# Performance work log

Hardware: AMD Instinct MI355X
Metric: run time of the kernel (lower is better)

The kernel has to match this reference:

```python
import jax, jax.numpy as jnp
import numpy as np


def _blur_kernel():
    # make_kernel([1,3,3,1]) -> outer product, normalized; * upsample_factor**2 (=4)
    k = np.array([1.0, 3.0, 3.0, 1.0], dtype=np.float32)
    k2 = np.outer(k, k)
    k2 /= k2.sum()
    k2 *= 4.0
    return jnp.asarray(k2)  # [4,4]


def setup_inputs() -> dict:
    key = jax.random.key(0)
    ks = jax.random.split(key, 6)
    B, Cin, Cout, H, W = 8, 128, 128, 128, 128
    style_dim, sd = 512, 32
    lin_out = Cin * (sd // 2) * (sd // 2)  # 128*16*16 = 32768
    return {
        "x": jax.random.normal(ks[0], (B, Cin, H, W), jnp.float32),
        "style": jax.random.normal(ks[1], (B, style_dim), jnp.float32),
        "weight": jax.random.normal(ks[2], (Cout, Cin, 3, 3), jnp.float32),
        "lin_w": jax.random.normal(ks[3], (lin_out, style_dim), jnp.float32),
        "lin_b": jnp.ones((lin_out,), jnp.float32),  # bias_init=1
        "convw_w": jax.random.normal(ks[4], (Cout, Cin, 3, 3), jnp.float32),
        "convw_b": jnp.zeros((Cout,), jnp.float32),
        "convb_w": jax.random.normal(ks[5], (Cout, Cin, 3, 3), jnp.float32),
        "convb_b": jnp.zeros((Cout,), jnp.float32),
    }


DN = ('NCHW', 'OIHW', 'NCHW')


def reference(x, style, weight, lin_w, lin_b, convw_w, convw_b, convb_w, convb_b):
    B, Cin, H, W = x.shape
    Cout, K = weight.shape[0], weight.shape[2]
    scale = 1.0 / np.sqrt(Cin * K * K)  # equalized-lr scale, fan_in = Cin*K*K
    w = scale * weight  # [Cout, Cin, K, K]; identical per-sample -> plain conv

    # F.conv_transpose2d(stride=2, padding=0) == dilated conv with flipped kernel
    out = jax.lax.conv_general_dilated(
        x, jnp.flip(w, (2, 3)), (1, 1), [(K - 1, K - 1)] * 2,
        lhs_dilation=(2, 2), dimension_numbers=DN)  # [B, Cout, 2H+1, 2W+1]

    # upfirdn2d blur with pad=(1,1): depthwise conv with flipped 4x4 kernel
    bk = _blur_kernel()
    bw = jnp.tile(jnp.flip(bk, (0, 1))[None, None], (Cout, 1, 1, 1))  # [Cout,1,4,4]
    out = jax.lax.conv_general_dilated(
        out, bw, (1, 1), [(1, 1), (1, 1)], feature_group_count=Cout,
        dimension_numbers=DN)  # [B, Cout, 2H, 2W]

    # InstanceNorm2d(affine=False), eps=1e-5, biased variance
    mu = out.mean((2, 3), keepdims=True)
    var = out.var((2, 3), keepdims=True)
    out = (out - mu) * jax.lax.rsqrt(var + 1e-5)
    Ho, Wo = out.shape[2], out.shape[3]

    # spatial_modulation_shared: EqualLinear (fused_lrelu) + View
    half = int(round(np.sqrt(lin_w.shape[0] // Cin)))  # spatial_dim // 2
    sd = 2 * half
    lscale = 1.0 / np.sqrt(style.shape[1])
    s = style @ (lin_w * lscale).T
    s = jax.nn.leaky_relu(s + lin_b, 0.2) * np.sqrt(2.0)  # fused_leaky_relu
    smap = s.reshape(B, Cin, half, half)
    # nn.Upsample(scale_factor=2, mode='nearest')
    smap = jnp.repeat(jnp.repeat(smap, 2, axis=2), 2, axis=3)  # [B,Cin,sd,sd]

    # two EqualConv2d(Cin, Cout, 3, padding=1)
    cscale = 1.0 / np.sqrt(Cin * 9)
    sw = jax.lax.conv_general_dilated(smap, convw_w * cscale, (1, 1),
                                      [(1, 1), (1, 1)], dimension_numbers=DN)
    sw = sw + convw_b[None, :, None, None]
    sb = jax.lax.conv_general_dilated(smap, convb_w * cscale, (1, 1),
                                      [(1, 1), (1, 1)], dimension_numbers=DN)
    sb = sb + convb_b[None, :, None, None]

    # F.interpolate(mode='nearest') to (Ho, Wo)
    hi = jnp.arange(Ho) * sd // Ho
    wi = jnp.arange(Wo) * sd // Wo
    sw = sw[:, :, hi][:, :, :, wi]
    sb = sb[:, :, hi][:, :, :, wi]

    return out * (1.0 + 0.3 * sw) + 0.3 * sb
```

## Files before the change

### kernel.cpp

```cpp
#include <hip/hip_runtime.h>
#include <cstdint>

#define SCALE_MAIN 0.029462782549439483f
#define LSCALE     0.044194173824159223f
#define CSCALE     0.029462782549439483f

typedef __attribute__((ext_vector_type(8))) short bf16x8;
typedef __attribute__((ext_vector_type(4))) float f32x4;
typedef __attribute__((ext_vector_type(4))) unsigned int u32x4;

static __device__ __forceinline__ float lrelu_s2(float v) {
  return (v > 0.f ? v : 0.2f * v) * 1.4142135623730951f;
}

static __device__ __forceinline__ unsigned short f2bf(float f) {
  unsigned int u = __builtin_bit_cast(unsigned int, f);
  u += 0x7FFFu + ((u >> 16) & 1u);
  return (unsigned short)(u >> 16);
}

__global__ __launch_bounds__(256) void keffb_kernel(const float* __restrict__ weight,
                                                    short* __restrict__ kb) {
  int idx = blockIdx.x * 256 + threadIdx.x;
  if (idx >= 128 * 128 * 36) return;
  int tap = idx % 9;
  int tmp = idx / 9;
  int par = tmp & 3;
  int cc  = tmp >> 2;
  int co = cc >> 7, ci = cc & 127;
  int ph = par >> 1, pw = par & 1;
  int a = tap / 3, b = tap % 3;
  int th = ph ? 3 - 2 * a : 2 - 2 * a;
  int tw = pw ? 3 - 2 * b : 2 - 2 * b;
  const float k4[4] = {1.f, 3.f, 3.f, 1.f};
  const float* wp = weight + cc * 9;
  float acc = 0.f;
  #pragma unroll
  for (int u = 0; u < 4; ++u) {
    int m = th - 1 + u;
    if (m < 0 || m > 2) continue;
    #pragma unroll
    for (int v = 0; v < 4; ++v) {
      int n = tw - 1 + v;
      if (n < 0 || n > 2) continue;
      acc += (k4[3 - u] * k4[3 - v] * (1.f / 16.f)) * wp[m * 3 + n];
    }
  }
  kb[(((par * 144) + tap * 16 + (ci >> 3)) * 128 + co) * 8 + (ci & 7)] =
      (short)f2bf(acc * SCALE_MAIN);
}

__global__ __launch_bounds__(256) void xpose_kernel(const float* __restrict__ x,
                                                    unsigned short* __restrict__ xt) {
  int y = blockIdx.x, b = blockIdx.y;
  __shared__ unsigned short tl[128 * 134];
  int t = threadIdx.x;
  #pragma unroll 4
  for (int i = 0; i < 16; ++i) {
    int c = t + i * 256;
    int ci = c >> 5, x4 = c & 31;
    f32x4 v = *(const f32x4*)(x + (size_t)(b * 128 + ci) * 16384 + y * 128 + x4 * 4);
    unsigned int* dst = (unsigned int*)(tl + ci * 134 + x4 * 4);
    dst[0] = (unsigned int)f2bf(v.x) | ((unsigned int)f2bf(v.y) << 16);
    dst[1] = (unsigned int)f2bf(v.z) | ((unsigned int)f2bf(v.w) << 16);
  }
  __syncthreads();
  #pragma unroll 2
  for (int i = 0; i < 8; ++i) {
    int c = t + i * 256;
    int xcol = c >> 4, sub = c & 15;
    unsigned short u[8];
    #pragma unroll
    for (int j = 0; j < 8; ++j) u[j] = tl[(sub * 8 + j) * 134 + xcol];
    u32x4 o;
    o.x = (unsigned int)u[0] | ((unsigned int)u[1] << 16);
    o.y = (unsigned int)u[2] | ((unsigned int)u[3] << 16);
    o.z = (unsigned int)u[4] | ((unsigned int)u[5] << 16);
    o.w = (unsigned int)u[6] | ((unsigned int)u[7] << 16);
    *(u32x4*)(xt + ((size_t)(b * 128 + y) * 128 + xcol) * 128 + sub * 8) = o;
  }
}

__global__ __launch_bounds__(256) void style_kernel(const float* __restrict__ style,
                                                    const float* __restrict__ lin_w,
                                                    const float* __restrict__ lin_b,
                                                    float* __restrict__ smap) {
  int wid = threadIdx.x >> 6, lane = threadIdx.x & 63;
  int gw = blockIdx.x * 4 + wid;
  const float4* st4 = (const float4*)style;
  float s[8][8];
  #pragma unroll
  for (int b = 0; b < 8; ++b) {
    float4 a0 = st4[b * 128 + lane * 2];
    float4 a1 = st4[b * 128 + lane * 2 + 1];
    s[b][0] = a0.x; s[b][1] = a0.y; s[b][2] = a0.z; s[b][3] = a0.w;
    s[b][4] = a1.x; s[b][5] = a1.y; s[b][6] = a1.z; s[b][7] = a1.w;
  }
  for (int rr = 0; rr < 16; ++rr) {
    int j = gw * 16 + rr;
    const float4* wp = (const float4*)(lin_w + (size_t)j * 512);
    float4 w0 = wp[lane * 2], w1 = wp[lane * 2 + 1];
    float acc[8];
    #pragma unroll
    for (int b = 0; b < 8; ++b) {
      acc[b] = w0.x * s[b][0] + w0.y * s[b][1] + w0.z * s[b][2] + w0.w * s[b][3]
             + w1.x * s[b][4] + w1.y * s[b][5] + w1.z * s[b][6] + w1.w * s[b][7];
    }
    #pragma unroll
    for (int m = 32; m; m >>= 1) {
      #pragma unroll
      for (int b = 0; b < 8; ++b) acc[b] += __shfl_xor(acc[b], m, 64);
    }
    if (lane == 0) {
      float bias = lin_b[j];
      #pragma unroll
      for (int b = 0; b < 8; ++b)
        smap[(size_t)b * 32768 + j] = lrelu_s2(acc[b] * LSCALE + bias);
    }
  }
}

__global__ __launch_bounds__(256) void modconv_kernel(const float* __restrict__ smap,
    const float* __restrict__ cw_w, const float* __restrict__ cw_b,
    const float* __restrict__ cb_w, const float* __restrict__ cb_b,
    float* __restrict__ sw, float* __restrict__ sb) {
  int co = blockIdx.x, b = blockIdx.y;
  int t = threadIdx.x;
  __shared__ float wts[2][1152];
  __shared__ float smc[8192];
  for (int i = t; i < 1152; i += 256) {
    wts[0][i] = cw_w[(size_t)co * 1152 + i];
    wts[1][i] = cb_w[(size_t)co * 1152 + i];
  }
  int qh = t >> 4, qw = t & 15;
  float aw[4] = {0, 0, 0, 0}, ab2[4] = {0, 0, 0, 0};
  for (int cc = 0; cc < 4; ++cc) {
    __syncthreads();
    const f32x4* sp4 = (const f32x4*)(smap + (size_t)b * 32768 + cc * 8192);
    f32x4* smc4 = (f32x4*)smc;
    #pragma unroll
    for (int i = 0; i < 8; ++i) smc4[t + i * 256] = sp4[t + i * 256];
    __syncthreads();
    for (int ci = 0; ci < 32; ++ci) {
      const float* sm = smc + ci * 256;
      float pt[3][3];
      #pragma unroll
      for (int dy = 0; dy < 3; ++dy)
      #pragma unroll
      for (int dx = 0; dx < 3; ++dx) {
        int yy = qh - 1 + dy, xx = qw - 1 + dx;
        pt[dy][dx] = (yy >= 0 && yy < 16 && xx >= 0 && xx < 16) ? sm[yy * 16 + xx] : 0.f;
      }
      const float* w0p = &wts[0][(cc * 32 + ci) * 9];
      const float* w1p = &wts[1][(cc * 32 + ci) * 9];
      #pragma unroll
      for (int kh = 0; kh < 3; ++kh)
      #pragma unroll
      for (int kw = 0; kw < 3; ++kw) {
        float wwv = w0p[kh * 3 + kw], wbv = w1p[kh * 3 + kw];
        #pragma unroll
        for (int q = 0; q < 4; ++q) {
          int ey = (q >> 1) - 1 + kh;
          int ex = (q & 1) - 1 + kw;
          int py = (ey < 0) ? 0 : (ey < 2 ? 1 : 2);
          int px = (ex < 0) ? 0 : (ex < 2 ? 1 : 2);
          float v = pt[py][px];
          aw[q] += wwv * v;
          ab2[q] += wbv * v;
        }
      }
    }
  }
  float bw = cw_b[co], bb = cb_b[co];
  #pragma unroll
  for (int q = 0; q < 4; ++q) {
    int h = 2 * qh + (q >> 1), w = 2 * qw + (q & 1);
    size_t o = ((size_t)(b * 128 + co) * 32 + h) * 32 + w;
    sw[o] = aw[q] * CSCALE + bw;
    sb[o] = ab2[q] * CSCALE + bb;
  }
}

#define LOADSTEP(S, AV, BV)                                                      \
  {                                                                              \
    int tap_ = (S) >> 2;                                                         \
    int ta_ = (tap_ * 11) >> 5, tb_ = tap_ - ta_ * 3;                            \
    const char* ab_ = abase + (ta_ * 66 + tb_) * 272 + ((S) & 3) * 64;           \
    _Pragma("unroll")                                                            \
    for (int mf = 0; mf < 4; ++mf) AV[mf] = *(const bf16x8*)(ab_ + mf * 4352);   \
    _Pragma("unroll")                                                            \
    for (int nf = 0; nf < 8; ++nf) BV[nf] = kbv[bbase + (S) * 512 + nf * 16];    \
  }
#define MFMASTEP(AV, BV)                                                         \
  _Pragma("unroll")                                                              \
  for (int nf = 0; nf < 8; ++nf)                                                 \
  _Pragma("unroll")                                                              \
  for (int mf = 0; mf < 4; ++mf)                                                 \
    acc[mf][nf] = __builtin_amdgcn_mfma_f32_16x16x32_bf16(AV[mf], BV[nf], acc[mf][nf], 0, 0, 0);

template <int BF16OUT>
__global__ __launch_bounds__(256, 2) void main_kernel(const unsigned short* __restrict__ xt,
    const short* __restrict__ kb, float* __restrict__ out,
    unsigned short* __restrict__ xout, float* __restrict__ partial) {
  __shared__ __align__(16) char smem[53856];
  int xh = blockIdx.x, y0 = blockIdx.y, b = blockIdx.z;
  int x0 = xh * 64;
  int t = threadIdx.x;
  int lane = t & 63, p = t >> 6;
  int m15 = lane & 15, ksub = lane >> 4;
  int ph = p >> 1, pw = p & 1;

  const char* xtc = (const char*)xt;
  for (int c = t; c < 3168; c += 256) {
    int spos = c >> 4, sub = c & 15;
    int aa = spos / 66, cc2 = spos - aa * 66;
    int y = y0 - 1 + aa, xg = x0 - 1 + cc2;
    f32x4 v = {0.f, 0.f, 0.f, 0.f};
    if ((unsigned)y < 128u && (unsigned)xg < 128u)
      v = *(const f32x4*)(xtc + ((size_t)((b * 128 + y) * 128 + xg)) * 256 + sub * 16);
    *(f32x4*)(smem + spos * 272 + sub * 16) = v;
  }
  __syncthreads();

  const bf16x8* kbv = (const bf16x8*)kb;
  int bbase = p * 18432 + ksub * 128 + m15;
  const char* abase = smem + m15 * 272 + ksub * 16;

  f32x4 acc[4][8];
  #pragma unroll
  for (int i = 0; i < 4; ++i)
  #pragma unroll
  for (int j = 0; j < 8; ++j) acc[i][j] = (f32x4){0.f, 0.f, 0.f, 0.f};

  bf16x8 avA[4], bvA[8], avB[4], bvB[8];
  LOADSTEP(0, avA, bvA)
  for (int s = 0; s < 36; s += 2) {
    LOADSTEP(s + 1, avB, bvB)
    MFMASTEP(avA, bvA)
    if (s + 2 < 36) LOADSTEP(s + 2, avA, bvA)
    MFMASTEP(avB, bvB)
  }

  __syncthreads();
  float* eps = (float*)smem;
  int co16 = t & 15, slotid = t >> 4;
  int ph2 = slotid >> 3, w16 = slotid & 7;
  #pragma unroll
  for (int r2 = 0; r2 < 4; ++r2) {
    #pragma unroll
    for (int e = 0; e < 2; ++e) {
      int nf = r2 * 2 + e;
      float s1 = 0.f, s2 = 0.f;
      #pragma unroll
      for (int mf = 0; mf < 4; ++mf)
      #pragma unroll
      for (int r = 0; r < 4; ++r) {
        int xx = mf * 16 + ksub * 4 + r;
        float v = acc[mf][nf][r];
        eps[((e * 2 + ph) * 128 + 2 * xx + pw) * 17 + m15] = v;
        s1 += v; s2 += v * v;
      }
      s1 += __shfl_xor(s1, 16, 64); s1 += __shfl_xor(s1, 32, 64);
      s2 += __shfl_xor(s2, 16, 64); s2 += __shfl_xor(s2, 32, 64);
      if (lane < 16) {
        int co = nf * 16 + lane;
        size_t pidx = (((((size_t)b * 128 + co) * 128 + y0) * 2 + xh) * 4 + p) * 2;
        partial[pidx] = s1; partial[pidx + 1] = s2;
      }
    }
    __syncthreads();
    #pragma unroll
    for (int e = 0; e < 2; ++e) {
      int nf = r2 * 2 + e;
      int co = nf * 16 + co16;
      int h = 2 * y0 + ph2;
      float vv[16];
      #pragma unroll
      for (int i = 0; i < 16; ++i)
        vv[i] = eps[((e * 2 + ph2) * 128 + w16 * 16 + i) * 17 + co16];
      size_t obase = ((size_t)(b * 128 + co) * 256 + h) * 256 + xh * 128 + w16 * 16;
      if (BF16OUT) {
        u32x4 o0, o1;
        o0.x = (unsigned int)f2bf(vv[0])  | ((unsigned int)f2bf(vv[1])  << 16);
        o0.y = (unsigned int)f2bf(vv[2])  | ((unsigned int)f2bf(vv[3])  << 16);
        o0.z = (unsigned int)f2bf(vv[4])  | ((unsigned int)f2bf(vv[5])  << 16);
        o0.w = (unsigned int)f2bf(vv[6])  | ((unsigned int)f2bf(vv[7])  << 16);
        o1.x = (unsigned int)f2bf(vv[8])  | ((unsigned int)f2bf(vv[9])  << 16);
        o1.y = (unsigned int)f2bf(vv[10]) | ((unsigned int)f2bf(vv[11]) << 16);
        o1.z = (unsigned int)f2bf(vv[12]) | ((unsigned int)f2bf(vv[13]) << 16);
        o1.w = (unsigned int)f2bf(vv[14]) | ((unsigned int)f2bf(vv[15]) << 16);
        *(u32x4*)(xout + obase) = o0;
        *(u32x4*)(xout + obase + 8) = o1;
      } else {
        #pragma unroll
        for (int i = 0; i < 4; ++i) {
          f32x4 o4 = {vv[i * 4], vv[i * 4 + 1], vv[i * 4 + 2], vv[i * 4 + 3]};
          *(f32x4*)(out + obase + i * 4) = o4;
        }
      }
    }
    __syncthreads();
  }
}

__global__ __launch_bounds__(256) void stats_kernel(const float* __restrict__ partial,
                                                    float* __restrict__ stats) {
  int bc = blockIdx.x;
  int t = threadIdx.x;
  float s1 = 0.f, s2 = 0.f;
  for (int j = t; j < 1024; j += 256) {
    s1 += partial[(size_t)bc * 2048 + 2 * j];
    s2 += partial[(size_t)bc * 2048 + 2 * j + 1];
  }
  #pragma unroll
  for (int m = 32; m; m >>= 1) { s1 += __shfl_xor(s1, m, 64); s2 += __shfl_xor(s2, m, 64); }
  __shared__ float rb[8];
  if ((t & 63) == 0) { rb[(t >> 6) * 2] = s1; rb[(t >> 6) * 2 + 1] = s2; }
  __syncthreads();
  if (t == 0) {
    float a1 = rb[0] + rb[2] + rb[4] + rb[6];
    float a2 = rb[1] + rb[3] + rb[5] + rb[7];
    float mean = a1 * (1.f / 65536.f);
    float var = a2 * (1.f / 65536.f) - mean * mean;
    stats[bc * 2] = mean;
    stats[bc * 2 + 1] = rsqrtf(var + 1e-5f);
  }
}

__global__ __launch_bounds__(256) void final_kernel(float* __restrict__ out,
    const float* __restrict__ sw, const float* __restrict__ sb,
    const float* __restrict__ stats) {
  unsigned int tid = blockIdx.x * 256 + threadIdx.x;
  unsigned int e = tid * 4;
  unsigned int w = e & 255u;
  unsigned int h = (e >> 8) & 255u;
  unsigned int bc = e >> 16;
  float mean = stats[bc * 2], rstd = stats[bc * 2 + 1];
  unsigned int sidx = (bc * 32 + (h >> 3)) * 32 + (w >> 3);
  float f1 = (1.f + 0.3f * sw[sidx]) * rstd;
  float f0 = 0.3f * sb[sidx] - mean * f1;
  float4 v = *(float4*)(out + e);
  v.x = v.x * f1 + f0;
  v.y = v.y * f1 + f0;
  v.z = v.z * f1 + f0;
  v.w = v.w * f1 + f0;
  *(float4*)(out + e) = v;
}

__global__ __launch_bounds__(256) void final_bf16_kernel(float* __restrict__ out,
    const unsigned short* __restrict__ xout,
    const float* __restrict__ sw, const float* __restrict__ sb,
    const float* __restrict__ stats) {
  unsigned int tid = blockIdx.x * 256 + threadIdx.x;
  unsigned int e = tid * 8;
  unsigned int w = e & 255u;
  unsigned int h = (e >> 8) & 255u;
  unsigned int bc = e >> 16;
  float mean = stats[bc * 2], rstd = stats[bc * 2 + 1];
  unsigned int sidx = (bc * 32 + (h >> 3)) * 32 + (w >> 3);
  float f1 = (1.f + 0.3f * sw[sidx]) * rstd;
  float f0 = 0.3f * sb[sidx] - mean * f1;
  u32x4 uv = *(const u32x4*)(xout + e);
  float o[8];
  #pragma unroll
  for (int j = 0; j < 4; ++j) {
    unsigned int word = uv[j];
    float lo = __builtin_bit_cast(float, word << 16);
    float hi = __builtin_bit_cast(float, word & 0xFFFF0000u);
    o[2 * j]     = lo * f1 + f0;
    o[2 * j + 1] = hi * f1 + f0;
  }
  f32x4 a = {o[0], o[1], o[2], o[3]}, c = {o[4], o[5], o[6], o[7]};
  *(f32x4*)(out + e) = a;
  *(f32x4*)(out + e + 4) = c;
}

extern "C" void kernel_launch(void* const* d_in, const int* in_sizes, int n_in,
                              void* d_out, int out_size, void* d_ws, size_t ws_size,
                              hipStream_t stream) {
  const float* x      = (const float*)d_in[0];
  const float* style  = (const float*)d_in[1];
  const float* weight = (const float*)d_in[2];
  const float* lin_w  = (const float*)d_in[3];
  const float* lin_b  = (const float*)d_in[4];
  const float* cw_w   = (const float*)d_in[5];
  const float* cw_b   = (const float*)d_in[6];
  const float* cb_w   = (const float*)d_in[7];
  const float* cb_b   = (const float*)d_in[8];
  float* out = (float*)d_out;
  char* ws = (char*)d_ws;

  short*          kbb   = (short*)(ws);
  unsigned short* xt    = (unsigned short*)(ws + 1179648);
  float*          smap  = (float*)(ws + 34734080);
  float*          swb   = (float*)(ws + 35782656);
  float*          sbb   = (float*)(ws + 39976960);
  float*          part  = (float*)(ws + 44171264);
  float*          stats = (float*)(ws + 52559872);
  unsigned short* xout  = (unsigned short*)(ws + 52568064);
  bool bigws = ws_size >= (size_t)186785792;

  keffb_kernel<<<dim3(2304), dim3(256), 0, stream>>>(weight, kbb);
  xpose_kernel<<<dim3(128, 8), dim3(256), 0, stream>>>(x, xt);
  style_kernel<<<dim3(512), dim3(256), 0, stream>>>(style, lin_w, lin_b, smap);
  modconv_kernel<<<dim3(128, 8), dim3(256), 0, stream>>>(smap, cw_w, cw_b, cb_w, cb_b, swb, sbb);
  if (bigws) {
    main_kernel<1><<<dim3(2, 128, 8), dim3(256), 0, stream>>>(xt, kbb, out, xout, part);
    stats_kernel<<<dim3(1024), dim3(256), 0, stream>>>(part, stats);
    final_bf16_kernel<<<dim3(32768), dim3(256), 0, stream>>>(out, xout, swb, sbb, stats);
  } else {
    main_kernel<0><<<dim3(2, 128, 8), dim3(256), 0, stream>>>(xt, kbb, out, nullptr, part);
    stats_kernel<<<dim3(1024), dim3(256), 0, stream>>>(part, stats);
    final_kernel<<<dim3(65536), dim3(256), 0, stream>>>(out, swb, sbb, stats);
  }
}
```

Baseline: 393.7 us.

## Rewrite style modulation conv as polyphase bf16 MFMA GEMM and prioritize MFMA issue

```diff
diff --git a/kernel.cpp b/kernel.cpp
--- a/kernel.cpp
+++ b/kernel.cpp
@@ -50,6 +50,38 @@
       (short)f2bf(acc * SCALE_MAIN);
 }
 
+__global__ __launch_bounds__(256) void kb2_kernel(const float* __restrict__ cw_w,
+                                                  const float* __restrict__ cb_w,
+                                                  short* __restrict__ kb2) {
+  int idx = blockIdx.x * 256 + threadIdx.x;
+  if (idx >= 524288) return;
+  int j   = idx & 7;
+  int co  = (idx >> 3) & 255;
+  int kc  = (idx >> 11) & 63;
+  int par = idx >> 17;
+  int k = kc * 8 + j;
+  int t2 = k >> 7, ci = k & 127;
+  int dy2 = t2 >> 1, dx2 = t2 & 1;
+  int ph = par >> 1, pw = par & 1;
+  const float* wsrc = (co < 128)
+      ? cw_w + ((size_t)co * 128 + ci) * 9
+      : cb_w + ((size_t)(co - 128) * 128 + ci) * 9;
+  float acc = 0.f;
+  #pragma unroll
+  for (int kh = 0; kh < 3; ++kh) {
+    bool okh = dy2 == 0 ? (ph == 0 ? kh == 0 : kh <= 1)
+                        : (ph == 0 ? kh >= 1 : kh == 2);
+    if (!okh) continue;
+    #pragma unroll
+    for (int kw = 0; kw < 3; ++kw) {
+      bool okw = dx2 == 0 ? (pw == 0 ? kw == 0 : kw <= 1)
+                          : (pw == 0 ? kw >= 1 : kw == 2);
+      if (okw) acc += wsrc[kh * 3 + kw];
+    }
+  }
+  kb2[idx] = (short)f2bf(acc * CSCALE);
+}
+
 __global__ __launch_bounds__(256) void xpose_kernel(const float* __restrict__ x,
                                                     unsigned short* __restrict__ xt) {
   int y = blockIdx.x, b = blockIdx.y;
@@ -84,7 +116,7 @@
 __global__ __launch_bounds__(256) void style_kernel(const float* __restrict__ style,
                                                     const float* __restrict__ lin_w,
                                                     const float* __restrict__ lin_b,
-                                                    float* __restrict__ smap) {
+                                                    unsigned short* __restrict__ smap_bf) {
   int wid = threadIdx.x >> 6, lane = threadIdx.x & 63;
   int gw = blockIdx.x * 4 + wid;
   const float4* st4 = (const float4*)style;
@@ -113,71 +145,79 @@
     }
     if (lane == 0) {
       float bias = lin_b[j];
+      int ci = j >> 8, sp = j & 255;
       #pragma unroll
       for (int b = 0; b < 8; ++b)
-        smap[(size_t)b * 32768 + j] = lrelu_s2(acc[b] * LSCALE + bias);
-    }
-  }
-}
-
-__global__ __launch_bounds__(256) void modconv_kernel(const float* __restrict__ smap,
-    const float* __restrict__ cw_w, const float* __restrict__ cw_b,
-    const float* __restrict__ cb_w, const float* __restrict__ cb_b,
-    float* __restrict__ sw, float* __restrict__ sb) {
-  int co = blockIdx.x, b = blockIdx.y;
-  int t = threadIdx.x;
-  __shared__ float wts[2][1152];
-  __shared__ float smc[8192];
-  for (int i = t; i < 1152; i += 256) {
-    wts[0][i] = cw_w[(size_t)co * 1152 + i];
-    wts[1][i] = cb_w[(size_t)co * 1152 + i];
-  }
-  int qh = t >> 4, qw = t & 15;
-  float aw[4] = {0, 0, 0, 0}, ab2[4] = {0, 0, 0, 0};
-  for (int cc = 0; cc < 4; ++cc) {
-    __syncthreads();
-    const f32x4* sp4 = (const f32x4*)(smap + (size_t)b * 32768 + cc * 8192);
-    f32x4* smc4 = (f32x4*)smc;
-    #pragma unroll
-    for (int i = 0; i < 8; ++i) smc4[t + i * 256] = sp4[t + i * 256];
-    __syncthreads();
-    for (int ci = 0; ci < 32; ++ci) {
-      const float* sm = smc + ci * 256;
-      float pt[3][3];
-      #pragma unroll
-      for (int dy = 0; dy < 3; ++dy)
-      #pragma unroll
-      for (int dx = 0; dx < 3; ++dx) {
-        int yy = qh - 1 + dy, xx = qw - 1 + dx;
-        pt[dy][dx] = (yy >= 0 && yy < 16 && xx >= 0 && xx < 16) ? sm[yy * 16 + xx] : 0.f;
+        smap_bf[(size_t)(b * 256 + sp) * 128 + ci] =
+            f2bf(lrelu_s2(acc[b] * LSCALE + bias));
+    }
+  }
+}
+
+__global__ __launch_bounds__(512, 2) void modconv_kernel(
+    const unsigned short* __restrict__ smap_bf, const short* __restrict__ kb2,
+    const float* __restrict__ cw_b, const float* __restrict__ cb_b,
+    float* __restrict__ swp) {
+  extern __shared__ __align__(16) char dsm[];
+  int par = blockIdx.x, b = blockIdx.y;
+  int ph = par >> 1, pw = par & 1;
+  int t = threadIdx.x, lane = t & 63, w = t >> 6;
+  int q = w >> 1, ch = w & 1;
+  int m15 = lane & 15, ksub = lane >> 4;
+
+  for (int c = t; c < 4624; c += 512) {
+    int s = c >> 4, cch = c & 15;
+    int rr = s / 17, cc = s - rr * 17;
+    int gr = rr - 1 + ph, gc = cc - 1 + pw;
+    u32x4 v = {0u, 0u, 0u, 0u};
+    if ((unsigned)gr < 16u && (unsigned)gc < 16u)
+      v = *(const u32x4*)(smap_bf + ((size_t)(b * 256 + gr * 16 + gc) * 128 + cch * 8));
+    int phys = (cch + s) & 15;
+    *(u32x4*)(dsm + s * 256 + phys * 16) = v;
+  }
+  __syncthreads();
+
+  const bf16x8* kbv = (const bf16x8*)kb2;
+  f32x4 acc[4][8];
+  #pragma unroll
+  for (int i = 0; i < 4; ++i)
+  #pragma unroll
+  for (int j = 0; j < 8; ++j) acc[i][j] = (f32x4){0.f, 0.f, 0.f, 0.f};
+
+  for (int s = 0; s < 16; ++s) {
+    int t2 = s >> 2, dy2 = t2 >> 1, dx2 = t2 & 1;
+    int cch = (s & 3) * 4 + ksub;
+    bf16x8 av[4];
+    #pragma unroll
+    for (int mf = 0; mf < 4; ++mf) {
+      int i = q * 4 + mf;
+      int ssp = (i + dy2) * 17 + (m15 + dx2);
+      int phys = (cch + ssp) & 15;
+      av[mf] = *(const bf16x8*)(dsm + ssp * 256 + phys * 16);
+    }
+    #pragma unroll
+    for (int nf = 0; nf < 8; ++nf) {
+      bf16x8 bv = kbv[(size_t)((par * 64 + s * 4 + ksub) * 256 + ch * 128 + nf * 16 + m15)];
+      #pragma unroll
+      for (int mf = 0; mf < 4; ++mf)
+        acc[mf][nf] = __builtin_amdgcn_mfma_f32_16x16x32_bf16(av[mf], bv, acc[mf][nf], 0, 0, 0);
+    }
+  }
+
+  int jbase = ksub * 4;
+  #pragma unroll
+  for (int nf = 0; nf < 8; ++nf) {
+    int co = ch * 128 + nf * 16 + m15;
+    float bias = (co < 128) ? cw_b[co] : cb_b[co - 128];
+    #pragma unroll
+    for (int mf = 0; mf < 4; ++mf) {
+      int i = q * 4 + mf;
+      #pragma unroll
+      for (int r = 0; r < 4; ++r) {
+        int px = i * 16 + jbase + r;
+        swp[((size_t)(b * 256 + co) * 4 + par) * 256 + px] = acc[mf][nf][r] + bias;
       }
-      const float* w0p = &wts[0][(cc * 32 + ci) * 9];
-      const float* w1p = &wts[1][(cc * 32 + ci) * 9];
-      #pragma unroll
-      for (int kh = 0; kh < 3; ++kh)
-      #pragma unroll
-      for (int kw = 0; kw < 3; ++kw) {
-        float wwv = w0p[kh * 3 + kw], wbv = w1p[kh * 3 + kw];
-        #pragma unroll
-        for (int q = 0; q < 4; ++q) {
-          int ey = (q >> 1) - 1 + kh;
-          int ex = (q & 1) - 1 + kw;
-          int py = (ey < 0) ? 0 : (ey < 2 ? 1 : 2);
-          int px = (ex < 0) ? 0 : (ex < 2 ? 1 : 2);
-          float v = pt[py][px];
-          aw[q] += wwv * v;
-          ab2[q] += wbv * v;
-        }
-      }
-    }
-  }
-  float bw = cw_b[co], bb = cb_b[co];
-  #pragma unroll
-  for (int q = 0; q < 4; ++q) {
-    int h = 2 * qh + (q >> 1), w = 2 * qw + (q & 1);
-    size_t o = ((size_t)(b * 128 + co) * 32 + h) * 32 + w;
-    sw[o] = aw[q] * CSCALE + bw;
-    sb[o] = ab2[q] * CSCALE + bb;
+    }
   }
 }
 
@@ -192,11 +232,13 @@
     for (int nf = 0; nf < 8; ++nf) BV[nf] = kbv[bbase + (S) * 512 + nf * 16];    \
   }
 #define MFMASTEP(AV, BV)                                                         \
+  __builtin_amdgcn_s_setprio(1);                                                 \
   _Pragma("unroll")                                                              \
   for (int nf = 0; nf < 8; ++nf)                                                 \
   _Pragma("unroll")                                                              \
   for (int mf = 0; mf < 4; ++mf)                                                 \
-    acc[mf][nf] = __builtin_amdgcn_mfma_f32_16x16x32_bf16(AV[mf], BV[nf], acc[mf][nf], 0, 0, 0);
+    acc[mf][nf] = __builtin_amdgcn_mfma_f32_16x16x32_bf16(AV[mf], BV[nf], acc[mf][nf], 0, 0, 0); \
+  __builtin_amdgcn_s_setprio(0);
 
 template <int BF16OUT>
 __global__ __launch_bounds__(256, 2) void main_kernel(const unsigned short* __restrict__ xt,
@@ -328,17 +370,21 @@
 }
 
 __global__ __launch_bounds__(256) void final_kernel(float* __restrict__ out,
-    const float* __restrict__ sw, const float* __restrict__ sb,
-    const float* __restrict__ stats) {
+    const float* __restrict__ swp, const float* __restrict__ stats) {
   unsigned int tid = blockIdx.x * 256 + threadIdx.x;
   unsigned int e = tid * 4;
   unsigned int w = e & 255u;
   unsigned int h = (e >> 8) & 255u;
   unsigned int bc = e >> 16;
+  unsigned int b = bc >> 7, co = bc & 127u;
   float mean = stats[bc * 2], rstd = stats[bc * 2 + 1];
-  unsigned int sidx = (bc * 32 + (h >> 3)) * 32 + (w >> 3);
-  float f1 = (1.f + 0.3f * sw[sidx]) * rstd;
-  float f0 = 0.3f * sb[sidx] - mean * f1;
+  unsigned int r32 = h >> 3, c32 = w >> 3;
+  unsigned int par = (r32 & 1u) * 2 + (c32 & 1u);
+  unsigned int px = (r32 >> 1) * 16 + (c32 >> 1);
+  float msw = swp[((size_t)(b * 256 + co) * 4 + par) * 256 + px];
+  float msb = swp[((size_t)(b * 256 + 128 + co) * 4 + par) * 256 + px];
+  float f1 = (1.f + 0.3f * msw) * rstd;
+  float f0 = 0.3f * msb - mean * f1;
   float4 v = *(float4*)(out + e);
   v.x = v.x * f1 + f0;
   v.y = v.y * f1 + f0;
@@ -349,17 +395,21 @@
 
 __global__ __launch_bounds__(256) void final_bf16_kernel(float* __restrict__ out,
     const unsigned short* __restrict__ xout,
-    const float* __restrict__ sw, const float* __restrict__ sb,
-    const float* __restrict__ stats) {
+    const float* __restrict__ swp, const float* __restrict__ stats) {
   unsigned int tid = blockIdx.x * 256 + threadIdx.x;
   unsigned int e = tid * 8;
   unsigned int w = e & 255u;
   unsigned int h = (e >> 8) & 255u;
   unsigned int bc = e >> 16;
+  unsigned int b = bc >> 7, co = bc & 127u;
   float mean = stats[bc * 2], rstd = stats[bc * 2 + 1];
-  unsigned int sidx = (bc * 32 + (h >> 3)) * 32 + (w >> 3);
-  float f1 = (1.f + 0.3f * sw[sidx]) * rstd;
-  float f0 = 0.3f * sb[sidx] - mean * f1;
+  unsigned int r32 = h >> 3, c32 = w >> 3;
+  unsigned int par = (r32 & 1u) * 2 + (c32 & 1u);
+  unsigned int px = (r32 >> 1) * 16 + (c32 >> 1);
+  float msw = swp[((size_t)(b * 256 + co) * 4 + par) * 256 + px];
+  float msb = swp[((size_t)(b * 256 + 128 + co) * 4 + par) * 256 + px];
+  float f1 = (1.f + 0.3f * msw) * rstd;
+  float f0 = 0.3f * msb - mean * f1;
   u32x4 uv = *(const u32x4*)(xout + e);
   float o[8];
   #pragma unroll
@@ -390,27 +440,28 @@
   float* out = (float*)d_out;
   char* ws = (char*)d_ws;
 
-  short*          kbb   = (short*)(ws);
-  unsigned short* xt    = (unsigned short*)(ws + 1179648);
-  float*          smap  = (float*)(ws + 34734080);
-  float*          swb   = (float*)(ws + 35782656);
-  float*          sbb   = (float*)(ws + 39976960);
-  float*          part  = (float*)(ws + 44171264);
-  float*          stats = (float*)(ws + 52559872);
-  unsigned short* xout  = (unsigned short*)(ws + 52568064);
+  short*          kbb     = (short*)(ws);
+  unsigned short* xt      = (unsigned short*)(ws + 1179648);
+  float*          swp     = (float*)(ws + 34734080);
+  float*          part    = (float*)(ws + 43122688);
+  short*          kb2     = (short*)(ws + 43122688);
+  unsigned short* smap_bf = (unsigned short*)(ws + 44171264);
+  float*          stats   = (float*)(ws + 51511296);
+  unsigned short* xout    = (unsigned short*)(ws + 51519488);
   bool bigws = ws_size >= (size_t)186785792;
 
   keffb_kernel<<<dim3(2304), dim3(256), 0, stream>>>(weight, kbb);
+  kb2_kernel<<<dim3(2048), dim3(256), 0, stream>>>(cw_w, cb_w, kb2);
   xpose_kernel<<<dim3(128, 8), dim3(256), 0, stream>>>(x, xt);
-  style_kernel<<<dim3(512), dim3(256), 0, stream>>>(style, lin_w, lin_b, smap);
-  modconv_kernel<<<dim3(128, 8), dim3(256), 0, stream>>>(smap, cw_w, cw_b, cb_w, cb_b, swb, sbb);
+  style_kernel<<<dim3(512), dim3(256), 0, stream>>>(style, lin_w, lin_b, smap_bf);
+  modconv_kernel<<<dim3(4, 8), dim3(512), 73984, stream>>>(smap_bf, kb2, cw_b, cb_b, swp);
   if (bigws) {
     main_kernel<1><<<dim3(2, 128, 8), dim3(256), 0, stream>>>(xt, kbb, out, xout, part);
     stats_kernel<<<dim3(1024), dim3(256), 0, stream>>>(part, stats);
-    final_bf16_kernel<<<dim3(32768), dim3(256), 0, stream>>>(out, xout, swb, sbb, stats);
+    final_bf16_kernel<<<dim3(32768), dim3(256), 0, stream>>>(out, xout, swp, stats);
   } else {
     main_kernel<0><<<dim3(2, 128, 8), dim3(256), 0, stream>>>(xt, kbb, out, nullptr, part);
     stats_kernel<<<dim3(1024), dim3(256), 0, stream>>>(part, stats);
-    final_kernel<<<dim3(65536), dim3(256), 0, stream>>>(out, swb, sbb, stats);
-  }
-}
+    final_kernel<<<dim3(65536), dim3(256), 0, stream>>>(out, swp, stats);
+  }
+}
```

Result: faster. 343.8 us (-12.7%).
